# Performance work log

Measured on AMD Instinct MI355X. Metric: run time of the kernel, lower is better.

Reference implementation:

```python
import jax, jax.numpy as jnp
import numpy as np

E = 4096      # hidden_size
H = 32        # num_attention_heads
D = E // H    # head_dim = 128
PAST = 8191   # past kv length


def setup_inputs() -> dict:
    key = jax.random.key(0)
    ks = jax.random.split(key, 10)
    s = 0.02
    return {
        "hidden_states": jax.random.normal(ks[0], (1, 1, E), jnp.float32),
        "past_key": jax.random.normal(ks[1], (1, D, PAST), jnp.float32),
        "past_value": jax.random.normal(ks[2], (1, PAST, D), jnp.float32),
        "attention_mask": jnp.zeros((1, 1, 1, PAST + 1), jnp.float32),
        "q_w": jax.random.normal(ks[3], (E, E), jnp.float32) * s,
        "q_b": jnp.zeros((E,), jnp.float32),
        "kv_w": jax.random.normal(ks[4], (E, 2 * D), jnp.float32) * s,
        "kv_b": jnp.zeros((2 * D,), jnp.float32),
        "proj_w": jax.random.normal(ks[5], (E, E), jnp.float32) * s,
        "proj_b": jnp.zeros((E,), jnp.float32),
    }


def reference(hidden_states, past_key, past_value, attention_mask,
              q_w, q_b, kv_w, kv_b, proj_w, proj_b):
    B, S = hidden_states.shape[:2]  # B=1, S=1 (decode)
    # Conv1D projections: x @ W + b
    query = hidden_states @ q_w + q_b            # [B, S, E]
    kv = hidden_states @ kv_w + kv_b             # [B, S, 2D]
    key_new, value_new = kv[..., :D], kv[..., D:]  # [B, S, D] each

    q = query.reshape(B, S, H, D).transpose(0, 2, 1, 3)  # [B, H, S, D]
    key_perm = key_new.transpose(0, 2, 1)                 # [B, D, S]
    full_key = jnp.concatenate([past_key, key_perm], axis=-1)     # [B, D, K]
    full_value = jnp.concatenate([past_value, value_new], axis=-2)  # [B, K, D]
    K = full_key.shape[-1]

    # QK^T with shared single KV head, scaled by sqrt(head_dim)
    scores = jnp.einsum('bhqd,bdk->bhqk', q, full_key)  # [B, H, S, K]
    scores = scores / jnp.asarray(D ** 0.5, scores.dtype)

    # causal mask over rows [K-S, K)
    causal = (jnp.arange(K)[None, :] <= (jnp.arange(S) + (K - S))[:, None])  # [S, K]
    mask_value = jnp.asarray(jnp.finfo(scores.dtype).min, scores.dtype)
    scores = jnp.where(causal[None, None], scores, mask_value)
    scores = scores + attention_mask

    attn_weights = jax.nn.softmax(scores, axis=-1)                # [B, H, S, K]
    attn_out = jnp.einsum('bhqk,bkd->bhqd', attn_weights, full_value)  # [B, H, S, D]
    attn_out = attn_out.transpose(0, 2, 1, 3).reshape(B, S, E)    # merge heads
    attn_out = attn_out @ proj_w + proj_b                          # [B, S, E]
    return attn_out, key_perm, value_new
```

## Files before the change

### kernel.cpp

```cpp
#include <hip/hip_runtime.h>
#include <math.h>

#define E_DIM 4096
#define H_NUM 32
#define D_DIM 128
#define PAST_K 8191
#define K_TOT 8192

#define WS_QUERY 0
#define WS_KV    4096
#define WS_L     4352
#define WS_ATTN  4416
#define WS_PQ    8512
#define WS_PA    (WS_PQ + 128*4352)
#define WS_PL    (WS_PA + 64*4096)
#define WS_PP    (WS_PL + 4096)

__global__ void k_qkv(const float* __restrict__ hs,
                      const float* __restrict__ q_w,
                      const float* __restrict__ kv_w,
                      float* __restrict__ ws) {
    const int t = threadIdx.x;
    const int e0 = blockIdx.y * 32;
    if (blockIdx.x < 4) {
        const int o = blockIdx.x * 1024 + t * 4;
        float ax = 0.f, ay = 0.f, az = 0.f, aw = 0.f;
#pragma unroll
        for (int i = 0; i < 32; ++i) {
            const int e = e0 + i;
            const float x = hs[e];
            const float4 w = *reinterpret_cast<const float4*>(q_w + (size_t)e * E_DIM + o);
            ax += x * w.x; ay += x * w.y; az += x * w.z; aw += x * w.w;
        }
        *reinterpret_cast<float4*>(ws + WS_PQ + (size_t)blockIdx.y * 4352 + o) =
            make_float4(ax, ay, az, aw);
    } else {
        if (t >= 64) return;
        const int o = t * 4;
        float ax = 0.f, ay = 0.f, az = 0.f, aw = 0.f;
#pragma unroll
        for (int i = 0; i < 32; ++i) {
            const int e = e0 + i;
            const float x = hs[e];
            const float4 w = *reinterpret_cast<const float4*>(kv_w + (size_t)e * 256 + o);
            ax += x * w.x; ay += x * w.y; az += x * w.z; aw += x * w.w;
        }
        *reinterpret_cast<float4*>(ws + WS_PQ + (size_t)blockIdx.y * 4352 + 4096 + o) =
            make_float4(ax, ay, az, aw);
    }
}

__global__ void k_qkv_reduce(const float* __restrict__ q_b, const float* __restrict__ kv_b,
                             float* __restrict__ ws) {
    const int o = blockIdx.x * 256 + threadIdx.x;
    float acc = 0.f;
#pragma unroll 8
    for (int s = 0; s < 128; ++s) acc += ws[WS_PQ + (size_t)s * 4352 + o];
    if (o < 4096) ws[WS_QUERY + o] = acc + q_b[o];
    else          ws[WS_KV + (o - 4096)] = acc + kv_b[o - 4096];
}

__global__ void __launch_bounds__(512, 4)
k_attn(const float* __restrict__ past_key,
       const float* __restrict__ past_value,
       const float* __restrict__ mask,
       float* __restrict__ ws,
       float* __restrict__ out) {
    __shared__ float sq[4 * 128];
    __shared__ float sp[4 * 128];
    __shared__ float red[16 * 128];
    const int t = threadIdx.x;
    const int hy = blockIdx.y;
    const int kx = blockIdx.x;
    const int h0 = hy * 4;
    const int k0 = kx * 128;
    const float* __restrict__ kvn = ws + WS_KV;

    sq[t % 512] = ws[WS_QUERY + h0 * D_DIM + (t % 512)];
    __syncthreads();

    const int kl = t & 127;
    const int team = t >> 7;
    const int d0 = team * 32;
    const int k = k0 + kl;
    const bool tailA = (k == PAST_K);
    const float* kp = tailA ? (kvn + d0) : (past_key + (size_t)d0 * PAST_K + k);
    const size_t kstr = tailA ? 1 : PAST_K;

    float a0 = 0.f, a1 = 0.f, a2 = 0.f, a3 = 0.f;
#pragma unroll
    for (int i = 0; i < 32; i += 4) {
        const float v0 = kp[0];
        const float v1 = kp[kstr];
        const float v2 = kp[2 * kstr];
        const float v3 = kp[3 * kstr];
        kp += 4 * kstr;
        const float4 q0 = *reinterpret_cast<const float4*>(&sq[0 * 128 + d0 + i]);
        const float4 q1 = *reinterpret_cast<const float4*>(&sq[1 * 128 + d0 + i]);
        const float4 q2 = *reinterpret_cast<const float4*>(&sq[2 * 128 + d0 + i]);
        const float4 q3 = *reinterpret_cast<const float4*>(&sq[3 * 128 + d0 + i]);
        a0 += q0.x * v0 + q0.y * v1 + q0.z * v2 + q0.w * v3;
        a1 += q1.x * v0 + q1.y * v1 + q1.z * v2 + q1.w * v3;
        a2 += q2.x * v0 + q2.y * v1 + q2.z * v2 + q2.w * v3;
        a3 += q3.x * v0 + q3.y * v1 + q3.z * v2 + q3.w * v3;
    }
    if (team != 0) {
        red[(team * 4 + 0) * 128 + kl] = a0;
        red[(team * 4 + 1) * 128 + kl] = a1;
        red[(team * 4 + 2) * 128 + kl] = a2;
        red[(team * 4 + 3) * 128 + kl] = a3;
    }
    __syncthreads();
    if (team == 0) {
        const float scale = 0.08838834764831845f;
        const float mk = mask[k];
        float s0 = a0, s1 = a1, s2 = a2, s3 = a3;
#pragma unroll
        for (int tm = 1; tm < 4; ++tm) {
            s0 += red[(tm * 4 + 0) * 128 + kl];
            s1 += red[(tm * 4 + 1) * 128 + kl];
            s2 += red[(tm * 4 + 2) * 128 + kl];
            s3 += red[(tm * 4 + 3) * 128 + kl];
        }
        const float e0 = __expf(s0 * scale + mk);
        const float e1 = __expf(s1 * scale + mk);
        const float e2 = __expf(s2 * scale + mk);
        const float e3 = __expf(s3 * scale + mk);
        sp[0 * 128 + kl] = e0;
        sp[1 * 128 + kl] = e1;
        sp[2 * 128 + kl] = e2;
        sp[3 * 128 + kl] = e3;
        float l0 = e0, l1 = e1, l2 = e2, l3 = e3;
#pragma unroll
        for (int off = 32; off > 0; off >>= 1) {
            l0 += __shfl_xor(l0, off);
            l1 += __shfl_xor(l1, off);
            l2 += __shfl_xor(l2, off);
            l3 += __shfl_xor(l3, off);
        }
        if ((t & 63) == 0) {
            const int w = t >> 6;
            float* pl = ws + WS_PL + ((size_t)(kx * 8 + hy)) * 8 + w * 4;
            pl[0] = l0; pl[1] = l1; pl[2] = l2; pl[3] = l3;
        }
    }
    __syncthreads();

    const int d = t & 127;
    const int kg = t >> 7;
    const int kb = k0 + kg * 32;
    const float* __restrict__ vp = past_value + (size_t)kb * D_DIM + d;
    const float* __restrict__ vlast =
        (kb + 31 == PAST_K) ? (kvn + D_DIM + d) : (vp + 31 * (size_t)D_DIM);

    float b0 = 0.f, b1 = 0.f, b2 = 0.f, b3 = 0.f;
#pragma unroll
    for (int kk = 0; kk < 31; ++kk) {
        const float v = vp[(size_t)kk * D_DIM];
        b0 += sp[0 * 128 + kg * 32 + kk] * v;
        b1 += sp[1 * 128 + kg * 32 + kk] * v;
        b2 += sp[2 * 128 + kg * 32 + kk] * v;
        b3 += sp[3 * 128 + kg * 32 + kk] * v;
    }
    {
        const float v = *vlast;
        b0 += sp[0 * 128 + kg * 32 + 31] * v;
        b1 += sp[1 * 128 + kg * 32 + 31] * v;
        b2 += sp[2 * 128 + kg * 32 + 31] * v;
        b3 += sp[3 * 128 + kg * 32 + 31] * v;
    }
    __syncthreads();
    red[(kg * 4 + 0) * 128 + d] = b0;
    red[(kg * 4 + 1) * 128 + d] = b1;
    red[(kg * 4 + 2) * 128 + d] = b2;
    red[(kg * 4 + 3) * 128 + d] = b3;
    __syncthreads();

    const int hh = t >> 7;
    const float s = red[(0 * 4 + hh) * 128 + d] + red[(1 * 4 + hh) * 128 + d] +
                    red[(2 * 4 + hh) * 128 + d] + red[(3 * 4 + hh) * 128 + d];
    ws[WS_PA + (size_t)kx * 4096 + (h0 + hh) * D_DIM + d] = s;

    if (kx == 0 && hy == 0 && t < 256) out[E_DIM + t] = kvn[t];
}

__global__ void k_attn_reduce(float* __restrict__ ws) {
    const int t = threadIdx.x;
    if (blockIdx.x < 16) {
        const int o = blockIdx.x * 256 + t;
        float acc = 0.f;
#pragma unroll 8
        for (int s = 0; s < 64; ++s) acc += ws[WS_PA + (size_t)s * 4096 + o];
        ws[WS_ATTN + o] = acc;
    } else if (t < 32) {
        const int hy = t >> 2, hh = t & 3;
        float acc = 0.f;
#pragma unroll 8
        for (int kx = 0; kx < 64; ++kx) {
            const float* pl = ws + WS_PL + ((size_t)(kx * 8 + hy)) * 8;
            acc += pl[hh] + pl[4 + hh];
        }
        ws[WS_L + t] = acc;
    }
}

__global__ void k_proj(const float* __restrict__ proj_w,
                       const float* __restrict__ ws, float* __restrict__ wsp) {
    const int t = threadIdx.x;
    const int o = blockIdx.x * 1024 + t * 4;
    const int e0 = blockIdx.y * 32;
    float ax = 0.f, ay = 0.f, az = 0.f, aw = 0.f;
#pragma unroll
    for (int i = 0; i < 32; ++i) {
        const int e = e0 + i;
        const float x = ws[WS_ATTN + e] / ws[WS_L + (e >> 7)];
        const float4 w = *reinterpret_cast<const float4*>(proj_w + (size_t)e * E_DIM + o);
        ax += x * w.x; ay += x * w.y; az += x * w.z; aw += x * w.w;
    }
    *reinterpret_cast<float4*>(wsp + WS_PP + (size_t)blockIdx.y * 4096 + o) =
        make_float4(ax, ay, az, aw);
}

__global__ void k_proj_reduce(const float* __restrict__ proj_b,
                              float* __restrict__ ws, float* __restrict__ out) {
    const int o = blockIdx.x * 256 + threadIdx.x;
    float acc = proj_b[o];
#pragma unroll 8
    for (int s = 0; s < 128; ++s) acc += ws[WS_PP + (size_t)s * 4096 + o];
    out[o] = acc;
}

extern "C" void kernel_launch(void* const* d_in, const int* in_sizes, int n_in,
                              void* d_out, int out_size, void* d_ws, size_t ws_size,
                              hipStream_t stream) {
    const float* hs      = (const float*)d_in[0];
    const float* past_k  = (const float*)d_in[1];
    const float* past_v  = (const float*)d_in[2];
    const float* mask    = (const float*)d_in[3];
    const float* q_w     = (const float*)d_in[4];
    const float* q_b     = (const float*)d_in[5];
    const float* kv_w    = (const float*)d_in[6];
    const float* kv_b    = (const float*)d_in[7];
    const float* proj_w  = (const float*)d_in[8];
    const float* proj_b  = (const float*)d_in[9];
    float* out = (float*)d_out;
    float* ws  = (float*)d_ws;

    k_qkv        <<<dim3(5, 128), dim3(256), 0, stream>>>(hs, q_w, kv_w, ws);
    k_qkv_reduce <<<dim3(17),     dim3(256), 0, stream>>>(q_b, kv_b, ws);
    k_attn       <<<dim3(64, 8),  dim3(512), 0, stream>>>(past_k, past_v, mask, ws, out);
    k_attn_reduce<<<dim3(17),     dim3(256), 0, stream>>>(ws);
    k_proj       <<<dim3(4, 128), dim3(256), 0, stream>>>(proj_w, ws, ws);
    k_proj_reduce<<<dim3(16),     dim3(256), 0, stream>>>(proj_b, ws, out);
}
```

Measured before the change: 213.4 us.

## Double split counts, fuse attention reduce into projection, parallelize reductions

Halves the per-block reduction depth in the QKV projection, the attention and the output projection, which doubles grid sizes so more blocks share the bandwidth-bound weight and KV streaming. The separate attention-reduce kernel is removed: each projection block now reduces its own 16 attention partials and the softmax denominators before the GEMV. The reduce kernels split their sum over four thread groups with a shared-memory combine, and the new kv output is written from the QKV reduce. The cost is larger partial buffers and repeated partial-sum and denominator reads across the four projection column blocks.

```diff
diff --git a/kernel.cpp b/kernel.cpp
--- a/kernel.cpp
+++ b/kernel.cpp
@@ -9,11 +9,9 @@
 
 #define WS_QUERY 0
 #define WS_KV    4096
-#define WS_L     4352
-#define WS_ATTN  4416
-#define WS_PQ    8512
-#define WS_PA    (WS_PQ + 128*4352)
-#define WS_PL    (WS_PA + 64*4096)
+#define WS_PQ    4608
+#define WS_PA    (WS_PQ + 256*4352)
+#define WS_PL    (WS_PA + 128*4096)
 #define WS_PP    (WS_PL + 4096)
 
 __global__ void k_qkv(const float* __restrict__ hs,
@@ -21,12 +19,12 @@
                       const float* __restrict__ kv_w,
                       float* __restrict__ ws) {
     const int t = threadIdx.x;
-    const int e0 = blockIdx.y * 32;
+    const int e0 = blockIdx.y * 16;
     if (blockIdx.x < 4) {
         const int o = blockIdx.x * 1024 + t * 4;
         float ax = 0.f, ay = 0.f, az = 0.f, aw = 0.f;
 #pragma unroll
-        for (int i = 0; i < 32; ++i) {
+        for (int i = 0; i < 16; ++i) {
             const int e = e0 + i;
             const float x = hs[e];
             const float4 w = *reinterpret_cast<const float4*>(q_w + (size_t)e * E_DIM + o);
@@ -39,7 +37,7 @@
         const int o = t * 4;
         float ax = 0.f, ay = 0.f, az = 0.f, aw = 0.f;
 #pragma unroll
-        for (int i = 0; i < 32; ++i) {
+        for (int i = 0; i < 16; ++i) {
             const int e = e0 + i;
             const float x = hs[e];
             const float4 w = *reinterpret_cast<const float4*>(kv_w + (size_t)e * 256 + o);
@@ -51,37 +49,53 @@
 }
 
 __global__ void k_qkv_reduce(const float* __restrict__ q_b, const float* __restrict__ kv_b,
-                             float* __restrict__ ws) {
-    const int o = blockIdx.x * 256 + threadIdx.x;
+                             float* __restrict__ ws, float* __restrict__ out) {
+    __shared__ float rr[256];
+    const int t = threadIdx.x;
+    const int ol = t & 63;
+    const int sg = t >> 6;
+    const int o = blockIdx.x * 64 + ol;
     float acc = 0.f;
 #pragma unroll 8
-    for (int s = 0; s < 128; ++s) acc += ws[WS_PQ + (size_t)s * 4352 + o];
-    if (o < 4096) ws[WS_QUERY + o] = acc + q_b[o];
-    else          ws[WS_KV + (o - 4096)] = acc + kv_b[o - 4096];
+    for (int s = sg * 64; s < sg * 64 + 64; ++s)
+        acc += ws[WS_PQ + (size_t)s * 4352 + o];
+    rr[sg * 64 + ol] = acc;
+    __syncthreads();
+    if (t < 64) {
+        float v = rr[ol] + rr[64 + ol] + rr[128 + ol] + rr[192 + ol];
+        const int oo = blockIdx.x * 64 + ol;
+        if (oo < 4096) {
+            ws[WS_QUERY + oo] = v + q_b[oo];
+        } else {
+            const int i = oo - 4096;
+            const float r = v + kv_b[i];
+            ws[WS_KV + i] = r;
+            out[oo] = r;
+        }
+    }
 }
 
 __global__ void __launch_bounds__(512, 4)
 k_attn(const float* __restrict__ past_key,
        const float* __restrict__ past_value,
        const float* __restrict__ mask,
-       float* __restrict__ ws,
-       float* __restrict__ out) {
+       float* __restrict__ ws) {
     __shared__ float sq[4 * 128];
-    __shared__ float sp[4 * 128];
-    __shared__ float red[16 * 128];
+    __shared__ float sp[4 * 64];
+    __shared__ float red[2048];
     const int t = threadIdx.x;
     const int hy = blockIdx.y;
     const int kx = blockIdx.x;
     const int h0 = hy * 4;
-    const int k0 = kx * 128;
+    const int k0 = kx * 64;
     const float* __restrict__ kvn = ws + WS_KV;
 
-    sq[t % 512] = ws[WS_QUERY + h0 * D_DIM + (t % 512)];
-    __syncthreads();
-
-    const int kl = t & 127;
-    const int team = t >> 7;
-    const int d0 = team * 32;
+    sq[t] = ws[WS_QUERY + h0 * D_DIM + t];
+    __syncthreads();
+
+    const int kl = t & 63;
+    const int team = t >> 6;
+    const int d0 = team * 16;
     const int k = k0 + kl;
     const bool tailA = (k == PAST_K);
     const float* kp = tailA ? (kvn + d0) : (past_key + (size_t)d0 * PAST_K + k);
@@ -89,7 +103,7 @@
 
     float a0 = 0.f, a1 = 0.f, a2 = 0.f, a3 = 0.f;
 #pragma unroll
-    for (int i = 0; i < 32; i += 4) {
+    for (int i = 0; i < 16; i += 4) {
         const float v0 = kp[0];
         const float v1 = kp[kstr];
         const float v2 = kp[2 * kstr];
@@ -105,10 +119,10 @@
         a3 += q3.x * v0 + q3.y * v1 + q3.z * v2 + q3.w * v3;
     }
     if (team != 0) {
-        red[(team * 4 + 0) * 128 + kl] = a0;
-        red[(team * 4 + 1) * 128 + kl] = a1;
-        red[(team * 4 + 2) * 128 + kl] = a2;
-        red[(team * 4 + 3) * 128 + kl] = a3;
+        red[((team - 1) * 4 + 0) * 64 + kl] = a0;
+        red[((team - 1) * 4 + 1) * 64 + kl] = a1;
+        red[((team - 1) * 4 + 2) * 64 + kl] = a2;
+        red[((team - 1) * 4 + 3) * 64 + kl] = a3;
     }
     __syncthreads();
     if (team == 0) {
@@ -116,20 +130,20 @@
         const float mk = mask[k];
         float s0 = a0, s1 = a1, s2 = a2, s3 = a3;
 #pragma unroll
-        for (int tm = 1; tm < 4; ++tm) {
-            s0 += red[(tm * 4 + 0) * 128 + kl];
-            s1 += red[(tm * 4 + 1) * 128 + kl];
-            s2 += red[(tm * 4 + 2) * 128 + kl];
-            s3 += red[(tm * 4 + 3) * 128 + kl];
+        for (int tm = 0; tm < 7; ++tm) {
+            s0 += red[(tm * 4 + 0) * 64 + kl];
+            s1 += red[(tm * 4 + 1) * 64 + kl];
+            s2 += red[(tm * 4 + 2) * 64 + kl];
+            s3 += red[(tm * 4 + 3) * 64 + kl];
         }
         const float e0 = __expf(s0 * scale + mk);
         const float e1 = __expf(s1 * scale + mk);
         const float e2 = __expf(s2 * scale + mk);
         const float e3 = __expf(s3 * scale + mk);
-        sp[0 * 128 + kl] = e0;
-        sp[1 * 128 + kl] = e1;
-        sp[2 * 128 + kl] = e2;
-        sp[3 * 128 + kl] = e3;
+        sp[0 * 64 + kl] = e0;
+        sp[1 * 64 + kl] = e1;
+        sp[2 * 64 + kl] = e2;
+        sp[3 * 64 + kl] = e3;
         float l0 = e0, l1 = e1, l2 = e2, l3 = e3;
 #pragma unroll
         for (int off = 32; off > 0; off >>= 1) {
@@ -138,9 +152,8 @@
             l2 += __shfl_xor(l2, off);
             l3 += __shfl_xor(l3, off);
         }
-        if ((t & 63) == 0) {
-            const int w = t >> 6;
-            float* pl = ws + WS_PL + ((size_t)(kx * 8 + hy)) * 8 + w * 4;
+        if (t == 0) {
+            float* pl = ws + WS_PL + ((size_t)(kx * 8 + hy)) * 4;
             pl[0] = l0; pl[1] = l1; pl[2] = l2; pl[3] = l3;
         }
     }
@@ -148,26 +161,26 @@
 
     const int d = t & 127;
     const int kg = t >> 7;
-    const int kb = k0 + kg * 32;
+    const int kb = k0 + kg * 16;
     const float* __restrict__ vp = past_value + (size_t)kb * D_DIM + d;
     const float* __restrict__ vlast =
-        (kb + 31 == PAST_K) ? (kvn + D_DIM + d) : (vp + 31 * (size_t)D_DIM);
+        (kb + 15 == PAST_K) ? (kvn + D_DIM + d) : (vp + 15 * (size_t)D_DIM);
 
     float b0 = 0.f, b1 = 0.f, b2 = 0.f, b3 = 0.f;
 #pragma unroll
-    for (int kk = 0; kk < 31; ++kk) {
+    for (int kk = 0; kk < 15; ++kk) {
         const float v = vp[(size_t)kk * D_DIM];
-        b0 += sp[0 * 128 + kg * 32 + kk] * v;
-        b1 += sp[1 * 128 + kg * 32 + kk] * v;
-        b2 += sp[2 * 128 + kg * 32 + kk] * v;
-        b3 += sp[3 * 128 + kg * 32 + kk] * v;
+        b0 += sp[0 * 64 + kg * 16 + kk] * v;
+        b1 += sp[1 * 64 + kg * 16 + kk] * v;
+        b2 += sp[2 * 64 + kg * 16 + kk] * v;
+        b3 += sp[3 * 64 + kg * 16 + kk] * v;
     }
     {
         const float v = *vlast;
-        b0 += sp[0 * 128 + kg * 32 + 31] * v;
-        b1 += sp[1 * 128 + kg * 32 + 31] * v;
-        b2 += sp[2 * 128 + kg * 32 + 31] * v;
-        b3 += sp[3 * 128 + kg * 32 + 31] * v;
+        b0 += sp[0 * 64 + kg * 16 + 15] * v;
+        b1 += sp[1 * 64 + kg * 16 + 15] * v;
+        b2 += sp[2 * 64 + kg * 16 + 15] * v;
+        b3 += sp[3 * 64 + kg * 16 + 15] * v;
     }
     __syncthreads();
     red[(kg * 4 + 0) * 128 + d] = b0;
@@ -180,54 +193,73 @@
     const float s = red[(0 * 4 + hh) * 128 + d] + red[(1 * 4 + hh) * 128 + d] +
                     red[(2 * 4 + hh) * 128 + d] + red[(3 * 4 + hh) * 128 + d];
     ws[WS_PA + (size_t)kx * 4096 + (h0 + hh) * D_DIM + d] = s;
-
-    if (kx == 0 && hy == 0 && t < 256) out[E_DIM + t] = kvn[t];
-}
-
-__global__ void k_attn_reduce(float* __restrict__ ws) {
-    const int t = threadIdx.x;
-    if (blockIdx.x < 16) {
-        const int o = blockIdx.x * 256 + t;
-        float acc = 0.f;
-#pragma unroll 8
-        for (int s = 0; s < 64; ++s) acc += ws[WS_PA + (size_t)s * 4096 + o];
-        ws[WS_ATTN + o] = acc;
-    } else if (t < 32) {
-        const int hy = t >> 2, hh = t & 3;
-        float acc = 0.f;
-#pragma unroll 8
-        for (int kx = 0; kx < 64; ++kx) {
-            const float* pl = ws + WS_PL + ((size_t)(kx * 8 + hy)) * 8;
-            acc += pl[hh] + pl[4 + hh];
-        }
-        ws[WS_L + t] = acc;
-    }
 }
 
 __global__ void k_proj(const float* __restrict__ proj_w,
-                       const float* __restrict__ ws, float* __restrict__ wsp) {
-    const int t = threadIdx.x;
+                       float* __restrict__ ws) {
+    __shared__ float sred[16 * 16];
+    __shared__ float lpart[2];
+    __shared__ float sa[16];
+    const int t = threadIdx.x;
+    const int by = blockIdx.y;
+    const int e0 = by * 16;
+    const int h  = by >> 3;
+    const int hy = h >> 2;
+    const int hh = h & 3;
+
+    {
+        const int el = t & 15;
+        const int kg = t >> 4;
+        float ps = 0.f;
+#pragma unroll
+        for (int j = 0; j < 8; ++j)
+            ps += ws[WS_PA + (size_t)(kg * 8 + j) * 4096 + e0 + el];
+        sred[kg * 16 + el] = ps;
+    }
+    if (t < 128) {
+        float lv = ws[WS_PL + ((size_t)(t * 8 + hy)) * 4 + hh];
+#pragma unroll
+        for (int off = 32; off > 0; off >>= 1) lv += __shfl_xor(lv, off);
+        if ((t & 63) == 0) lpart[t >> 6] = lv;
+    }
+    __syncthreads();
+    if (t < 16) {
+        float asum = 0.f;
+#pragma unroll
+        for (int g = 0; g < 16; ++g) asum += sred[g * 16 + t];
+        sa[t] = asum / (lpart[0] + lpart[1]);
+    }
+    __syncthreads();
+
     const int o = blockIdx.x * 1024 + t * 4;
-    const int e0 = blockIdx.y * 32;
     float ax = 0.f, ay = 0.f, az = 0.f, aw = 0.f;
 #pragma unroll
-    for (int i = 0; i < 32; ++i) {
-        const int e = e0 + i;
-        const float x = ws[WS_ATTN + e] / ws[WS_L + (e >> 7)];
-        const float4 w = *reinterpret_cast<const float4*>(proj_w + (size_t)e * E_DIM + o);
+    for (int i = 0; i < 16; ++i) {
+        const float x = sa[i];
+        const float4 w = *reinterpret_cast<const float4*>(proj_w + (size_t)(e0 + i) * E_DIM + o);
         ax += x * w.x; ay += x * w.y; az += x * w.z; aw += x * w.w;
     }
-    *reinterpret_cast<float4*>(wsp + WS_PP + (size_t)blockIdx.y * 4096 + o) =
+    *reinterpret_cast<float4*>(ws + WS_PP + (size_t)by * 4096 + o) =
         make_float4(ax, ay, az, aw);
 }
 
 __global__ void k_proj_reduce(const float* __restrict__ proj_b,
                               float* __restrict__ ws, float* __restrict__ out) {
-    const int o = blockIdx.x * 256 + threadIdx.x;
-    float acc = proj_b[o];
+    __shared__ float rr[256];
+    const int t = threadIdx.x;
+    const int ol = t & 63;
+    const int sg = t >> 6;
+    const int o = blockIdx.x * 64 + ol;
+    float acc = 0.f;
 #pragma unroll 8
-    for (int s = 0; s < 128; ++s) acc += ws[WS_PP + (size_t)s * 4096 + o];
-    out[o] = acc;
+    for (int s = sg * 64; s < sg * 64 + 64; ++s)
+        acc += ws[WS_PP + (size_t)s * 4096 + o];
+    rr[sg * 64 + ol] = acc;
+    __syncthreads();
+    if (t < 64) {
+        const int oo = blockIdx.x * 64 + ol;
+        out[oo] = rr[ol] + rr[64 + ol] + rr[128 + ol] + rr[192 + ol] + proj_b[oo];
+    }
 }
 
 extern "C" void kernel_launch(void* const* d_in, const int* in_sizes, int n_in,
@@ -246,10 +278,9 @@
     float* out = (float*)d_out;
     float* ws  = (float*)d_ws;
 
-    k_qkv        <<<dim3(5, 128), dim3(256), 0, stream>>>(hs, q_w, kv_w, ws);
-    k_qkv_reduce <<<dim3(17),     dim3(256), 0, stream>>>(q_b, kv_b, ws);
-    k_attn       <<<dim3(64, 8),  dim3(512), 0, stream>>>(past_k, past_v, mask, ws, out);
-    k_attn_reduce<<<dim3(17),     dim3(256), 0, stream>>>(ws);
-    k_proj       <<<dim3(4, 128), dim3(256), 0, stream>>>(proj_w, ws, ws);
-    k_proj_reduce<<<dim3(16),     dim3(256), 0, stream>>>(proj_b, ws, out);
-}
+    k_qkv        <<<dim3(5, 256), dim3(256), 0, stream>>>(hs, q_w, kv_w, ws);
+    k_qkv_reduce <<<dim3(68),     dim3(256), 0, stream>>>(q_b, kv_b, ws, out);
+    k_attn       <<<dim3(128, 8), dim3(512), 0, stream>>>(past_k, past_v, mask, ws);
+    k_proj       <<<dim3(4, 256), dim3(256), 0, stream>>>(proj_w, ws);
+    k_proj_reduce<<<dim3(64),     dim3(256), 0, stream>>>(proj_b, ws, out);
+}
```

Result: faster. 201.1 us (-5.7%).
